# Kernel optimization log

Hardware: AMD Instinct MI355X
Metric: run time of the kernel (lower is better)

Reference implementation:

```python
import jax, jax.numpy as jnp
import numpy as np

B, T, I, H, O = 1024, 512, 64, 256, 1


def setup_inputs() -> dict:
    key = jax.random.key(0)
    ks = jax.random.split(key, 7)
    s_ih = 1.0 / np.sqrt(H)
    return {
        "input_seq": jax.random.normal(ks[0], (B, T, I), dtype=jnp.float32),
        "W_ih": jax.random.uniform(ks[1], (4 * H, I), jnp.float32, -s_ih, s_ih),
        "W_hh": jax.random.uniform(ks[2], (4 * H, H), jnp.float32, -s_ih, s_ih),
        "b_ih": jax.random.uniform(ks[3], (4 * H,), jnp.float32, -s_ih, s_ih),
        "b_hh": jax.random.uniform(ks[4], (4 * H,), jnp.float32, -s_ih, s_ih),
        "W_out": jax.random.uniform(ks[5], (O, H), jnp.float32, -s_ih, s_ih),
        "b_out": jax.random.uniform(ks[6], (O,), jnp.float32, -s_ih, s_ih),
    }


def reference(input_seq, W_ih, W_hh, b_ih, b_hh, W_out, b_out):
    batch = input_seq.shape[0]
    hid = W_hh.shape[1]
    h0 = jnp.zeros((batch, hid), dtype=input_seq.dtype)
    c0 = jnp.zeros((batch, hid), dtype=input_seq.dtype)

    def step(carry, x_t):
        h, c = carry
        # PyTorch LSTMCell gate order: i, f, g, o
        gates = x_t @ W_ih.T + b_ih + h @ W_hh.T + b_hh  # [B, 4H]
        i, f, g, o = jnp.split(gates, 4, axis=-1)
        i = jax.nn.sigmoid(i)
        f = jax.nn.sigmoid(f)
        g = jnp.tanh(g)
        o = jax.nn.sigmoid(o)
        c_new = f * c + i * g
        h_new = o * jnp.tanh(c_new)
        return (h_new, c_new), None

    xs = jnp.swapaxes(input_seq, 0, 1)  # [T, B, I]
    (h_last, _), _ = jax.lax.scan(step, (h0, c0), xs)
    return h_last @ W_out.T + b_out  # [B, O]
```

## Files before the change

kernel.cpp:

```cpp
#include <hip/hip_runtime.h>
#include <hip/hip_bf16.h>


typedef float f32x4 __attribute__((ext_vector_type(4)));
typedef short s16x8 __attribute__((ext_vector_type(8)));

#define TT 512
#define II 64
#define HH 256

__device__ __forceinline__ ushort f2bf(float f) {
  unsigned u = __builtin_bit_cast(unsigned, f);
  u = (u + 0x7FFFu + ((u >> 16) & 1u)) >> 16;
  return (ushort)u;
}

__device__ __forceinline__ float sigm(float x) {
  return 1.0f / (1.0f + __expf(-x));
}
__device__ __forceinline__ float tanh_s(float x) {
  float e = __expf(-2.0f * fabsf(x));
  float t = (1.0f - e) / (1.0f + e);
  return copysignf(t, x);
}

__device__ __forceinline__ s16x8 pack_bf8(const float* p) {
  f32x4 a = *(const f32x4*)p;
  f32x4 b = *(const f32x4*)(p + 4);
  s16x8 r;
  r[0] = (short)f2bf(a[0]); r[1] = (short)f2bf(a[1]);
  r[2] = (short)f2bf(a[2]); r[3] = (short)f2bf(a[3]);
  r[4] = (short)f2bf(b[0]); r[5] = (short)f2bf(b[1]);
  r[6] = (short)f2bf(b[2]); r[7] = (short)f2bf(b[3]);
  return r;
}

__global__ __launch_bounds__(1024, 4) void lstm_one(
    const float* __restrict__ x,
    const float* __restrict__ wih_f,
    const float* __restrict__ whh_f,
    const float* __restrict__ b_ih,
    const float* __restrict__ b_hh,
    const float* __restrict__ w_out,
    const float* __restrict__ b_out,
    float* __restrict__ out)
{
  __shared__ ushort h_lds[2][16 * 256];
  __shared__ float hf[16][256];

  const int tid  = threadIdx.x;
  const int wv   = tid >> 6;
  const int l    = tid & 63;
  const int lrow = l & 15;
  const int lk8  = (l >> 4) << 3;
  const int crow = (l >> 4) << 2;
  const int ccol = l & 15;
  const int b0   = blockIdx.x << 4;
  const int col0 = wv << 4;

  s16x8 whh[4][8];
  s16x8 wih[4][2];
  float bs[4];
#pragma unroll
  for (int g = 0; g < 4; ++g) {
    const int wrow = g * 256 + col0 + lrow;
#pragma unroll
    for (int kf = 0; kf < 8; ++kf)
      whh[g][kf] = pack_bf8(whh_f + wrow * HH + kf * 32 + lk8);
#pragma unroll
    for (int kf = 0; kf < 2; ++kf)
      wih[g][kf] = pack_bf8(wih_f + wrow * II + kf * 32 + lk8);
    const int c = g * 256 + col0 + ccol;
    bs[g] = b_ih[c] + b_hh[c];
  }

  float cst[4] = {0.f, 0.f, 0.f, 0.f};

  f32x4 accn[4];
  {
    const float* xp = x + (size_t)(b0 + lrow) * TT * II + lk8;
    s16x8 x0 = pack_bf8(xp);
    s16x8 x1 = pack_bf8(xp + 32);
#pragma unroll
    for (int g = 0; g < 4; ++g) {
      f32x4 a;
      a[0] = a[1] = a[2] = a[3] = bs[g];
      a = __builtin_amdgcn_mfma_f32_16x16x32_bf16(x0, wih[g][0], a, 0, 0, 0);
      a = __builtin_amdgcn_mfma_f32_16x16x32_bf16(x1, wih[g][1], a, 0, 0, 0);
      accn[g] = a;
    }
  }

  for (int t = 0; t < TT; ++t) {
    s16x8 hfr[8];
    if (t > 0) {
#pragma unroll
      for (int kf = 0; kf < 8; ++kf) {
        int byte = (lrow * 512 + (kf * 32 + lk8) * 2) ^ ((lrow & 7) << 4);
        hfr[kf] = *(const s16x8*)((const char*)h_lds[t & 1] + byte);
      }
    }

    s16x8 xn0, xn1;
    if (t < TT - 1) {
      const float* xp = x + ((size_t)(b0 + lrow) * TT + (t + 1)) * II + lk8;
      xn0 = pack_bf8(xp);
      xn1 = pack_bf8(xp + 32);
    }

    f32x4 acc[4];
#pragma unroll
    for (int g = 0; g < 4; ++g) {
      f32x4 a = accn[g];
      if (t > 0) {
#pragma unroll
        for (int kf = 0; kf < 8; ++kf)
          a = __builtin_amdgcn_mfma_f32_16x16x32_bf16(hfr[kf], whh[g][kf], a,
                                                      0, 0, 0);
      }
      acc[g] = a;
    }

    if (t < TT - 1) {
#pragma unroll
      for (int g = 0; g < 4; ++g) {
        f32x4 a;
        a[0] = a[1] = a[2] = a[3] = bs[g];
        a = __builtin_amdgcn_mfma_f32_16x16x32_bf16(xn0, wih[g][0], a, 0, 0, 0);
        a = __builtin_amdgcn_mfma_f32_16x16x32_bf16(xn1, wih[g][1], a, 0, 0, 0);
        accn[g] = a;
      }
    }

#pragma unroll
    for (int r = 0; r < 4; ++r) {
      float gi = sigm(acc[0][r]);
      float gf = sigm(acc[1][r]);
      float gg = tanh_s(acc[2][r]);
      float go = sigm(acc[3][r]);
      float cn = gf * cst[r] + gi * gg;
      cst[r] = cn;
      float hn = go * tanh_s(cn);
      int row = crow + r;
      int col = col0 + ccol;
      if (t == TT - 1) {
        hf[row][col] = hn;
      } else {
        int byte = (row * 512 + col * 2) ^ ((row & 7) << 4);
        *(ushort*)((char*)h_lds[(t + 1) & 1] + byte) = f2bf(hn);
      }
    }

    __syncthreads();
  }

  {
    float s = hf[wv][l] * w_out[l] + hf[wv][l + 64] * w_out[l + 64] +
              hf[wv][l + 128] * w_out[l + 128] +
              hf[wv][l + 192] * w_out[l + 192];
#pragma unroll
    for (int off = 32; off >= 1; off >>= 1) s += __shfl_xor(s, off);
    if (l == 0) out[b0 + wv] = s + b_out[0];
  }
}

extern "C" void kernel_launch(void* const* d_in, const int* in_sizes, int n_in,
                              void* d_out, int out_size, void* d_ws, size_t ws_size,
                              hipStream_t stream) {
  const float* x     = (const float*)d_in[0];
  const float* wih   = (const float*)d_in[1];
  const float* whh   = (const float*)d_in[2];
  const float* b_ih  = (const float*)d_in[3];
  const float* b_hh  = (const float*)d_in[4];
  const float* w_out = (const float*)d_in[5];
  const float* b_out = (const float*)d_in[6];
  float* out = (float*)d_out;

  lstm_one<<<64, 1024, 0, stream>>>(x, wih, whh, b_ih, b_hh, w_out, b_out, out);
}
```

Measured before the change: 8.790 ms.

## Split each batch group's hidden dimension across two cooperating blocks with global flag sync

Each 16-row batch group is now handled by two 512-thread blocks, each owning half of the hidden units, so 128 blocks run instead of 64 and the per-step gate work per block is halved. The two halves exchange bf16 h through a global workspace buffer each step and synchronise with acquire/release counters and spin-waits. The final projection is combined with atomicAdd after a zero-init kernel. A fallback kernel is used when the workspace or CU count is insufficient. The cost is a cross-block global-memory handshake on every timestep, and the spin-wait relies on both blocks being resident at the same time.

```diff
diff --git a/kernel.cpp b/kernel.cpp
--- a/kernel.cpp
+++ b/kernel.cpp
@@ -5,9 +5,11 @@
 typedef float f32x4 __attribute__((ext_vector_type(4)));
 typedef short s16x8 __attribute__((ext_vector_type(8)));
 
+#define BB 1024
 #define TT 512
 #define II 64
 #define HH 256
+#define GG 1024
 
 __device__ __forceinline__ ushort f2bf(float f) {
   unsigned u = __builtin_bit_cast(unsigned, f);
@@ -35,7 +37,13 @@
   return r;
 }
 
-__global__ __launch_bounds__(1024, 4) void lstm_one(
+__global__ void init_kernel(float* __restrict__ out, unsigned* __restrict__ cnt) {
+  int i = blockIdx.x * 256 + threadIdx.x;
+  if (i < 1024) out[i] = 0.0f;
+  if (i < 2048) cnt[i] = 0u;
+}
+
+__global__ __launch_bounds__(512, 2) void lstm_pair(
     const float* __restrict__ x,
     const float* __restrict__ wih_f,
     const float* __restrict__ whh_f,
@@ -43,10 +51,12 @@
     const float* __restrict__ b_hh,
     const float* __restrict__ w_out,
     const float* __restrict__ b_out,
+    unsigned* __restrict__ cnt,
+    ushort* __restrict__ hx,
     float* __restrict__ out)
 {
-  __shared__ ushort h_lds[2][16 * 256];
-  __shared__ float hf[16][256];
+  __shared__ ushort h_lds[16 * 128];
+  __shared__ float hf[16][128];
 
   const int tid  = threadIdx.x;
   const int wv   = tid >> 6;
@@ -55,82 +65,86 @@
   const int lk8  = (l >> 4) << 3;
   const int crow = (l >> 4) << 2;
   const int ccol = l & 15;
-  const int b0   = blockIdx.x << 4;
-  const int col0 = wv << 4;
+  const int grp  = blockIdx.x & 63;
+  const int half = blockIdx.x >> 6;
+  const int b0   = grp << 4;
+  const int lc   = (wv << 4) + ccol;
+  const int hc0  = half << 7;
 
   s16x8 whh[4][8];
   s16x8 wih[4][2];
   float bs[4];
 #pragma unroll
   for (int g = 0; g < 4; ++g) {
-    const int wrow = g * 256 + col0 + lrow;
+    const int wrow = g * 256 + hc0 + (wv << 4) + lrow;
 #pragma unroll
     for (int kf = 0; kf < 8; ++kf)
       whh[g][kf] = pack_bf8(whh_f + wrow * HH + kf * 32 + lk8);
 #pragma unroll
     for (int kf = 0; kf < 2; ++kf)
       wih[g][kf] = pack_bf8(wih_f + wrow * II + kf * 32 + lk8);
-    const int c = g * 256 + col0 + ccol;
+    const int c = g * 256 + hc0 + (wv << 4) + ccol;
     bs[g] = b_ih[c] + b_hh[c];
   }
 
   float cst[4] = {0.f, 0.f, 0.f, 0.f};
 
-  f32x4 accn[4];
+  unsigned* mycnt = cnt + (((grp << 1) + half) << 4);
+  unsigned* pcnt  = cnt + (((grp << 1) + (1 - half)) << 4);
+
+  s16x8 xf[2];
   {
-    const float* xp = x + (size_t)(b0 + lrow) * TT * II + lk8;
-    s16x8 x0 = pack_bf8(xp);
-    s16x8 x1 = pack_bf8(xp + 32);
+    const float* xp = x + ((size_t)(b0 + lrow) * TT) * II + lk8;
+    xf[0] = pack_bf8(xp);
+    xf[1] = pack_bf8(xp + 32);
+  }
+
+  for (int t = 0; t < TT; ++t) {
+    s16x8 hown[4], hrem[4];
+    if (t > 0) {
+      while (__hip_atomic_load(pcnt, __ATOMIC_ACQUIRE,
+                               __HIP_MEMORY_SCOPE_AGENT) < (unsigned)t)
+        __builtin_amdgcn_s_sleep(1);
+      const ushort* rb = hx + ((size_t)(((t & 1) * 64 + grp) * 16 + lrow)) * 256
+                         + (1 - half) * 128 + lk8;
+#pragma unroll
+      for (int kf = 0; kf < 4; ++kf)
+        hrem[kf] = *(const s16x8*)(rb + kf * 32);
+#pragma unroll
+      for (int kf = 0; kf < 4; ++kf) {
+        int byte = (lrow * 256 + (kf * 32 + lk8) * 2) ^ ((lrow & 7) << 4);
+        hown[kf] = *(const s16x8*)((const char*)h_lds + byte);
+      }
+    }
+
+    s16x8 xfn[2];
+    if (t < TT - 1) {
+      const float* xp = x + ((size_t)(b0 + lrow) * TT + (t + 1)) * II + lk8;
+      xfn[0] = pack_bf8(xp);
+      xfn[1] = pack_bf8(xp + 32);
+    }
+
+    f32x4 acc[4];
 #pragma unroll
     for (int g = 0; g < 4; ++g) {
       f32x4 a;
       a[0] = a[1] = a[2] = a[3] = bs[g];
-      a = __builtin_amdgcn_mfma_f32_16x16x32_bf16(x0, wih[g][0], a, 0, 0, 0);
-      a = __builtin_amdgcn_mfma_f32_16x16x32_bf16(x1, wih[g][1], a, 0, 0, 0);
-      accn[g] = a;
-    }
-  }
-
-  for (int t = 0; t < TT; ++t) {
-    s16x8 hfr[8];
-    if (t > 0) {
-#pragma unroll
-      for (int kf = 0; kf < 8; ++kf) {
-        int byte = (lrow * 512 + (kf * 32 + lk8) * 2) ^ ((lrow & 7) << 4);
-        hfr[kf] = *(const s16x8*)((const char*)h_lds[t & 1] + byte);
-      }
-    }
-
-    s16x8 xn0, xn1;
-    if (t < TT - 1) {
-      const float* xp = x + ((size_t)(b0 + lrow) * TT + (t + 1)) * II + lk8;
-      xn0 = pack_bf8(xp);
-      xn1 = pack_bf8(xp + 32);
-    }
-
-    f32x4 acc[4];
-#pragma unroll
-    for (int g = 0; g < 4; ++g) {
-      f32x4 a = accn[g];
+      a = __builtin_amdgcn_mfma_f32_16x16x32_bf16(xf[0], wih[g][0], a, 0, 0, 0);
+      a = __builtin_amdgcn_mfma_f32_16x16x32_bf16(xf[1], wih[g][1], a, 0, 0, 0);
       if (t > 0) {
 #pragma unroll
-        for (int kf = 0; kf < 8; ++kf)
-          a = __builtin_amdgcn_mfma_f32_16x16x32_bf16(hfr[kf], whh[g][kf], a,
-                                                      0, 0, 0);
+        for (int kf = 0; kf < 4; ++kf)
+          a = __builtin_amdgcn_mfma_f32_16x16x32_bf16(hown[kf],
+                whh[g][half * 4 + kf], a, 0, 0, 0);
+#pragma unroll
+        for (int kf = 0; kf < 4; ++kf)
+          a = __builtin_amdgcn_mfma_f32_16x16x32_bf16(hrem[kf],
+                whh[g][(1 - half) * 4 + kf], a, 0, 0, 0);
       }
       acc[g] = a;
     }
 
-    if (t < TT - 1) {
-#pragma unroll
-      for (int g = 0; g < 4; ++g) {
-        f32x4 a;
-        a[0] = a[1] = a[2] = a[3] = bs[g];
-        a = __builtin_amdgcn_mfma_f32_16x16x32_bf16(xn0, wih[g][0], a, 0, 0, 0);
-        a = __builtin_amdgcn_mfma_f32_16x16x32_bf16(xn1, wih[g][1], a, 0, 0, 0);
-        accn[g] = a;
-      }
-    }
+    if (t > 0) __syncthreads();
 
 #pragma unroll
     for (int r = 0; r < 4; ++r) {
@@ -142,25 +156,126 @@
       cst[r] = cn;
       float hn = go * tanh_s(cn);
       int row = crow + r;
-      int col = col0 + ccol;
       if (t == TT - 1) {
-        hf[row][col] = hn;
+        hf[row][lc] = hn;
       } else {
+        ushort hb = f2bf(hn);
+        int byte = (row * 256 + lc * 2) ^ ((row & 7) << 4);
+        *(ushort*)((char*)h_lds + byte) = hb;
+        hx[((size_t)((((t + 1) & 1) * 64 + grp) * 16 + row)) * 256 + hc0 + lc] = hb;
+      }
+    }
+
+    if (t < TT - 1) {
+      __syncthreads();
+      if (tid == 0)
+        __hip_atomic_store(mycnt, (unsigned)(t + 1), __ATOMIC_RELEASE,
+                           __HIP_MEMORY_SCOPE_AGENT);
+    }
+    xf[0] = xfn[0];
+    xf[1] = xfn[1];
+  }
+
+  __syncthreads();
+  {
+    const int row = wv << 1;
+#pragma unroll
+    for (int rr = 0; rr < 2; ++rr) {
+      float s = hf[row + rr][l] * w_out[hc0 + l] +
+                hf[row + rr][l + 64] * w_out[hc0 + l + 64];
+#pragma unroll
+      for (int off = 32; off >= 1; off >>= 1) s += __shfl_xor(s, off);
+      if (l == 0)
+        atomicAdd(out + b0 + row + rr, s + (half == 0 ? b_out[0] : 0.f));
+    }
+  }
+}
+
+__global__ __launch_bounds__(512, 2) void lstm_fallback(
+    const float* __restrict__ x, const float* __restrict__ wih_f,
+    const float* __restrict__ whh_f, const float* __restrict__ b_ih,
+    const float* __restrict__ b_hh, const float* __restrict__ w_out,
+    const float* __restrict__ b_out, float* __restrict__ out) {
+  __shared__ ushort h_lds[16 * 256];
+  __shared__ float hf[16][256];
+  const int tid = threadIdx.x, wv = tid >> 6, l = tid & 63;
+  const int lrow = l & 15, lk8 = (l >> 4) << 3, crow = (l >> 4) << 2, ccol = l & 15;
+  const int b0 = blockIdx.x << 4, jw = wv << 5;
+  { s16x8 z = {}; *(s16x8*)&h_lds[tid * 8] = z; }
+  s16x8 wihf[4][2][2];
+#pragma unroll
+  for (int g = 0; g < 4; ++g)
+#pragma unroll
+    for (int nt = 0; nt < 2; ++nt)
+#pragma unroll
+      for (int kt = 0; kt < 2; ++kt)
+        wihf[g][nt][kt] = pack_bf8(wih_f + (g * 256 + jw + nt * 16 + lrow) * II + kt * 32 + lk8);
+  float bs[4][2];
+#pragma unroll
+  for (int g = 0; g < 4; ++g)
+#pragma unroll
+    for (int nt = 0; nt < 2; ++nt) {
+      int c = g * 256 + jw + nt * 16 + ccol;
+      bs[g][nt] = b_ih[c] + b_hh[c];
+    }
+  float cst[2][4] = {};
+  __syncthreads();
+  for (int t = 0; t < TT; ++t) {
+    s16x8 xf[2];
+    {
+      const float* xp = x + ((size_t)(b0 + lrow) * TT + t) * II + lk8;
+      xf[0] = pack_bf8(xp); xf[1] = pack_bf8(xp + 32);
+    }
+    s16x8 hfr[8];
+#pragma unroll
+    for (int kt = 0; kt < 8; ++kt) {
+      int byte = (lrow * 512 + (kt * 32 + lk8) * 2) ^ ((lrow & 7) << 4);
+      hfr[kt] = *(const s16x8*)((const char*)h_lds + byte);
+    }
+    f32x4 acc[4][2];
+#pragma unroll
+    for (int g = 0; g < 4; ++g)
+#pragma unroll
+      for (int nt = 0; nt < 2; ++nt) {
+        f32x4 a; a[0] = a[1] = a[2] = a[3] = bs[g][nt];
+        s16x8 bw[8];
+        int jrow = g * 256 + jw + nt * 16 + lrow;
+#pragma unroll
+        for (int kt = 0; kt < 8; ++kt)
+          bw[kt] = pack_bf8(whh_f + jrow * HH + kt * 32 + lk8);
+        a = __builtin_amdgcn_mfma_f32_16x16x32_bf16(xf[0], wihf[g][nt][0], a, 0, 0, 0);
+        a = __builtin_amdgcn_mfma_f32_16x16x32_bf16(xf[1], wihf[g][nt][1], a, 0, 0, 0);
+#pragma unroll
+        for (int kt = 0; kt < 8; ++kt)
+          a = __builtin_amdgcn_mfma_f32_16x16x32_bf16(hfr[kt], bw[kt], a, 0, 0, 0);
+        acc[g][nt] = a;
+      }
+    __syncthreads();
+#pragma unroll
+    for (int nt = 0; nt < 2; ++nt)
+#pragma unroll
+      for (int r = 0; r < 4; ++r) {
+        float gi = sigm(acc[0][nt][r]), gf = sigm(acc[1][nt][r]);
+        float gg = tanh_s(acc[2][nt][r]), go = sigm(acc[3][nt][r]);
+        float cn = gf * cst[nt][r] + gi * gg;
+        cst[nt][r] = cn;
+        float hn = go * tanh_s(cn);
+        int row = crow + r, col = jw + nt * 16 + ccol;
         int byte = (row * 512 + col * 2) ^ ((row & 7) << 4);
-        *(ushort*)((char*)h_lds[(t + 1) & 1] + byte) = f2bf(hn);
-      }
-    }
-
+        *(ushort*)((char*)h_lds + byte) = f2bf(hn);
+        if (t == TT - 1) hf[row][col] = hn;
+      }
     __syncthreads();
   }
-
-  {
-    float s = hf[wv][l] * w_out[l] + hf[wv][l + 64] * w_out[l + 64] +
-              hf[wv][l + 128] * w_out[l + 128] +
-              hf[wv][l + 192] * w_out[l + 192];
+#pragma unroll
+  for (int rr = 0; rr < 2; ++rr) {
+    int row = wv * 2 + rr;
+    float s = 0.f;
+#pragma unroll
+    for (int m = 0; m < 4; ++m) s += hf[row][l + 64 * m] * w_out[l + 64 * m];
 #pragma unroll
     for (int off = 32; off >= 1; off >>= 1) s += __shfl_xor(s, off);
-    if (l == 0) out[b0 + wv] = s + b_out[0];
+    if (l == 0) out[b0 + row] = s + b_out[0];
   }
 }
 
@@ -176,5 +291,19 @@
   const float* b_out = (const float*)d_in[6];
   float* out = (float*)d_out;
 
-  lstm_one<<<64, 1024, 0, stream>>>(x, wih, whh, b_ih, b_hh, w_out, b_out, out);
-}
+  int dev = 0, nCU = 0;
+  hipGetDevice(&dev);
+  hipDeviceGetAttribute(&nCU, hipDeviceAttributeMultiprocessorCount, dev);
+
+  const size_t ws_needed = 8192 + (size_t)2 * 64 * 16 * 256 * sizeof(ushort);
+  if (ws_size >= ws_needed && nCU >= 128) {
+    unsigned* cnt = (unsigned*)d_ws;
+    ushort* hx = (ushort*)((char*)d_ws + 8192);
+    init_kernel<<<8, 256, 0, stream>>>(out, cnt);
+    lstm_pair<<<128, 512, 0, stream>>>(x, wih, whh, b_ih, b_hh, w_out, b_out,
+                                       cnt, hx, out);
+  } else {
+    lstm_fallback<<<64, 512, 0, stream>>>(x, wih, whh, b_ih, b_hh, w_out, b_out,
+                                          out);
+  }
+}
```

Measured after the change: 10.72 ms. 1.22x slower.
